# Optimization experiments

Hardware: AMD Instinct MI355X
Metric: run time of the kernel (lower is better)

Reference implementation:

```python
import jax, jax.numpy as jnp
import numpy as np

IH, IW = 32, 32
HEADS, DIM_HEAD = 8, 32
EPS = 1e-6


def conv3x3(x, w):
    # x: [B,C,H,W], w: [O,I,3,3], stride 1, pad 1, no bias
    return jax.lax.conv_general_dilated(x, w, (1, 1), ((1, 1), (1, 1)),
                                        dimension_numbers=('NCHW', 'OIHW', 'NCHW'))


def groupnorm1(x, g, b):
    # GroupNorm(1, C): normalize over (C,H,W) per sample
    mu = jnp.mean(x, axis=(1, 2, 3), keepdims=True)
    var = jnp.var(x, axis=(1, 2, 3), keepdims=True)
    xn = (x - mu) * jax.lax.rsqrt(var + EPS)
    return xn * g[None, :, None, None] + b[None, :, None, None]


def proj(x, w, g, b):
    return jax.nn.gelu(groupnorm1(conv3x3(x, w), g, b), approximate=False)


def relative_index(ih, iw):
    coords = np.stack(np.meshgrid(np.arange(ih), np.arange(iw), indexing='ij')).reshape(2, -1)
    rel = coords[:, :, None] - coords[:, None, :]  # [2, n, n]
    rel[0] += ih - 1
    rel[1] += iw - 1
    rel[0] *= 2 * iw - 1
    return jnp.asarray(rel.sum(0).reshape(-1))  # [n*n]


def setup_inputs() -> dict:
    key = jax.random.key(0)
    ks = jax.random.split(key, 9)
    C = HEADS * DIM_HEAD  # 256
    B = 8
    s = 0.02
    inp = {
        'x': jax.random.normal(ks[0], (B, C, IH, IW), jnp.float32),
        'wq': jax.random.normal(ks[1], (C, C, 3, 3), jnp.float32) * s,
        'wk': jax.random.normal(ks[2], (C, C, 3, 3), jnp.float32) * s,
        'wv': jax.random.normal(ks[3], (C, C, 3, 3), jnp.float32) * s,
        'gq': jnp.ones((C,), jnp.float32), 'bq': jnp.zeros((C,), jnp.float32),
        'gk': jnp.ones((C,), jnp.float32), 'bk': jnp.zeros((C,), jnp.float32),
        'gv': jnp.ones((C,), jnp.float32), 'bv': jnp.zeros((C,), jnp.float32),
        'bias_table': jax.random.normal(ks[4], ((2 * IH - 1) * (2 * IW - 1), HEADS), jnp.float32) * s,
        'wo': jax.random.normal(ks[5], (C, C), jnp.float32) * s,
        'bo': jnp.zeros((C,), jnp.float32),
    }
    return inp


def reference(x, wq, wk, wv, gq, bq, gk, bk, gv, bv, bias_table, wo, bo):
    B, C, ih, iw = x.shape
    n = ih * iw
    h, d = HEADS, DIM_HEAD

    q = proj(x, wq, gq, bq)  # [B,C,H,W]
    k = proj(x, wk, gk, bk)
    v = proj(x, wv, gv, bv)

    # 'b c ih iw -> b (ih iw) c' then 'b n (h d) -> b h n d'  ==  [B,h,d,n] -> [B,h,n,d]
    def to_heads(t):
        return t.reshape(B, h, d, n).transpose(0, 1, 3, 2)

    q4, k4, v4 = to_heads(q), to_heads(k), to_heads(v)

    # NOTE: original code applies self.scale only when y is not None; y=None here -> no scale.
    dots = jnp.einsum('bhnd,bhmd->bhnm', q4, k4)  # [B,h,n,n]

    rel_idx = relative_index(ih, iw)  # [n*n]
    rel_bias = bias_table[rel_idx].reshape(n, n, h).transpose(2, 0, 1)[None]  # [1,h,n,n]

    attn = jax.nn.softmax(dots + rel_bias, axis=-1)
    out = jnp.einsum('bhnm,bhmd->bhnd', attn, v4)  # [B,h,n,d]

    # 'b h n d -> b n (h d)' then 'b (ih iw) c -> b c ih iw'
    out = out.transpose(0, 2, 1, 3).reshape(B, n, C).transpose(0, 2, 1).reshape(B, C, ih, iw)

    # to_out: 1x1 conv with bias (dropout=0 in eval)
    out = jnp.einsum('oc,bchw->bohw', wo, out) + bo[None, :, None, None]
    return out
```

## Files before the change

### kernel.cpp

```cpp
#include <hip/hip_runtime.h>
#include <cstdint>
#include <cstddef>

#define GEPS 1e-6f

using bf16x8 = __attribute__((ext_vector_type(8))) short;
using f32x4  = __attribute__((ext_vector_type(4))) float;

__device__ inline ushort f2bf(float x) {
    union { float f; uint32_t u; } v; v.f = x;
    uint32_t r = (v.u + 0x7fffu + ((v.u >> 16) & 1u)) >> 16;
    return (ushort)r;
}

__device__ inline void gll16(const void* g, void* l) {
    __builtin_amdgcn_global_load_lds(
        (const __attribute__((address_space(1))) void*)g,
        (__attribute__((address_space(3))) void*)l, 16, 0, 0);
}

__global__ __launch_bounds__(256) void pack_k(
    const float* __restrict__ wq, const float* __restrict__ wk,
    const float* __restrict__ wv, const float* __restrict__ wo,
    const float* __restrict__ btab,
    ushort* __restrict__ Wbuf, ushort* __restrict__ wo_bf,
    float* __restrict__ bias_r)
{
    int blk = blockIdx.x, tid = threadIdx.x;
    if (blk < 768) {
        __shared__ ushort Ws[2304];
        int proj = blk >> 8, co = blk & 255;
        const float* src = ((proj == 0) ? wq : ((proj == 1) ? wk : wv)) + (size_t)co * 2304;
#pragma unroll
        for (int j = 0; j < 9; ++j) {
            int idx = j * 256 + tid;
            Ws[idx] = f2bf(src[idx]);
        }
        __syncthreads();
        ushort* dst = Wbuf + (size_t)blk * 2304;
#pragma unroll
        for (int j = 0; j < 9; ++j)
            dst[j * 256 + tid] = Ws[tid * 9 + j];
        return;
    }
    if (blk < 832) {
        int t = (blk - 768) * 256 + tid;
        float4 v = *(const float4*)&wo[(size_t)t * 4];
        union { uint2 u; ushort s[4]; } o;
        o.s[0] = f2bf(v.x); o.s[1] = f2bf(v.y); o.s[2] = f2bf(v.z); o.s[3] = f2bf(v.w);
        *(uint2*)&wo_bf[(size_t)t * 4] = o.u;
        return;
    }
    int t = (blk - 832) * 256 + tid;
    if (t < 8 * 3969) {
        int h = t / 3969, rk = t - h * 3969;
        bias_r[t] = btab[rk * 8 + h];
    }
}

__global__ __launch_bounds__(256) void im2col_k(const float* __restrict__ x,
                                                ushort* __restrict__ Ab)
{
    __shared__ __align__(16) ushort Xs[3 * 34 * 128];
    int tid = threadIdx.x;
    int blk = blockIdx.x;
    int b = blk >> 6, py = (blk >> 1) & 31, half = blk & 1;

#pragma unroll
    for (int p = tid; p < 768; p += 256) {
        int yy = p >> 8;
        int q = p & 255;
        int col = (q >> 7) ? 33 : 0;
        int ci = q & 127;
        Xs[(yy * 34 + col) * 128 + ci] = 0;
    }

#pragma unroll
    for (int it = 0; it < 12; ++it) {
        int j = it * 256 + tid;
        int ci_l = j / 24;
        int o = (j - ci_l * 24) * 4;
        int yy = o >> 5, xx = o & 31;
        int row = py - 1 + yy;
        float4 v = make_float4(0.f, 0.f, 0.f, 0.f);
        if (row >= 0 && row < 32)
            v = *(const float4*)&x[((size_t)(b * 256 + half * 128 + ci_l)) * 1024 + row * 32 + xx];
        int base = (yy * 34 + xx + 1) * 128 + ci_l;
        Xs[base + 0 * 128] = f2bf(v.x);
        Xs[base + 1 * 128] = f2bf(v.y);
        Xs[base + 2 * 128] = f2bf(v.z);
        Xs[base + 3 * 128] = f2bf(v.w);
    }
    __syncthreads();

    ushort* dst = Ab + (size_t)(b * 1024 + py * 32) * 2304;
#pragma unroll
    for (int it = 0; it < 18; ++it) {
        int idx = it * 256 + tid;
        int ci8l = idx & 15;
        int tp = (idx >> 4) % 9;
        int px = idx / 144;
        int kh = tp / 3, kw = tp - kh * 3;
        uint4 p = *(const uint4*)&Xs[(kh * 34 + px + kw) * 128 + ci8l * 8];
        *(uint4*)&dst[(size_t)(px * 288 + tp * 32 + half * 16 + ci8l) * 8] = p;
    }
}

__global__ __launch_bounds__(256, 3) void gemm_bt(
    const ushort* __restrict__ A, const ushort* __restrict__ B,
    int M, int N, int K,
    float* __restrict__ Cpart,
    float* __restrict__ Cout, const float* __restrict__ bias, int mode)
{
    __shared__ __align__(16) ushort As[128 * 64];
    __shared__ __align__(16) ushort Bs[128 * 64];
    int tid = threadIdx.x;
    int mbase = blockIdx.x * 128, nbase = blockIdx.y * 128;
    int kspan = K / gridDim.z;
    int k0 = blockIdx.z * kspan;
    int wave = tid >> 6, lane = tid & 63;
    int wm = wave & 1, wn = wave >> 1;
    int quad = lane >> 4, c = lane & 15;

    int row_s = tid >> 3;
    int cc8 = (tid & 7) ^ (row_s & 7);
    ushort* ldsA = As + wave * 512;
    ushort* ldsB = Bs + wave * 512;

    f32x4 acc[4][4];
#pragma unroll
    for (int i = 0; i < 4; ++i)
#pragma unroll
        for (int j = 0; j < 4; ++j) acc[i][j] = (f32x4){0.f, 0.f, 0.f, 0.f};

    for (int kb = k0; kb < k0 + kspan; kb += 64) {
        __syncthreads();
#pragma unroll
        for (int R = 0; R < 4; ++R) {
            int row = R * 32 + row_s;
            gll16(A + (size_t)(mbase + row) * K + kb + cc8 * 8,
                  ldsA + R * 2048);
            gll16(B + (size_t)(nbase + row) * K + kb + cc8 * 8,
                  ldsB + R * 2048);
        }
        __syncthreads();
#pragma unroll
        for (int kq = 0; kq < 2; ++kq) {
            bf16x8 af[4], bfr[4];
            int sw = ((kq * 4 + quad) ^ (c & 7)) * 8;
#pragma unroll
            for (int i = 0; i < 4; ++i) {
                af[i]  = *(const bf16x8*)&As[(wm * 64 + i * 16 + c) * 64 + sw];
                bfr[i] = *(const bf16x8*)&Bs[(wn * 64 + i * 16 + c) * 64 + sw];
            }
#pragma unroll
            for (int i = 0; i < 4; ++i)
#pragma unroll
                for (int j = 0; j < 4; ++j)
                    acc[i][j] = __builtin_amdgcn_mfma_f32_16x16x32_bf16(
                        af[i], bfr[j], acc[i][j], 0, 0, 0);
        }
    }

    if (mode == 0) {
        float* Cp = Cpart + (size_t)blockIdx.z * M * N;
#pragma unroll
        for (int i = 0; i < 4; ++i) {
            int mrow = mbase + wm * 64 + i * 16 + quad * 4;
#pragma unroll
            for (int j = 0; j < 4; ++j) {
                int ncol = nbase + wn * 64 + j * 16 + c;
#pragma unroll
                for (int r = 0; r < 4; ++r)
                    Cp[(size_t)(mrow + r) * N + ncol] = acc[i][j][r];
            }
        }
    } else {
#pragma unroll
        for (int i = 0; i < 4; ++i) {
            int mrow0 = mbase + wm * 64 + i * 16 + quad * 4;
#pragma unroll
            for (int j = 0; j < 4; ++j) {
                int ncol = nbase + wn * 64 + j * 16 + c;
                int bb = ncol >> 10, px = ncol & 1023;
#pragma unroll
                for (int r = 0; r < 4; ++r) {
                    int o = mrow0 + r;
                    Cout[((size_t)bb * 256 + o) * 1024 + px] = acc[i][j][r] + bias[o];
                }
            }
        }
    }
}

__global__ __launch_bounds__(256) void stats1_k(const float* __restrict__ P0,
                                                const float* __restrict__ P1,
                                                float2* __restrict__ part)
{
    int t = blockIdx.x * 256 + threadIdx.x;
    size_t base = (size_t)t * 8;
    float4 a0 = *(const float4*)&P0[base];
    float4 a1 = *(const float4*)&P0[base + 4];
    float4 c0 = *(const float4*)&P1[base];
    float4 c1 = *(const float4*)&P1[base + 4];
    float v[8] = {a0.x + c0.x, a0.y + c0.y, a0.z + c0.z, a0.w + c0.w,
                  a1.x + c1.x, a1.y + c1.y, a1.z + c1.z, a1.w + c1.w};
    float s1 = 0.f, s2 = 0.f;
#pragma unroll
    for (int e = 0; e < 8; ++e) { s1 += v[e]; s2 += v[e] * v[e]; }
#pragma unroll
    for (int mk = 1; mk < 32; mk <<= 1) {
        s1 += __shfl_xor(s1, mk, 64);
        s2 += __shfl_xor(s2, mk, 64);
    }
    if ((threadIdx.x & 31) == 0) {
        int gg = t >> 5;
        int m = gg / 3;
        int proj = gg - m * 3;
        int b = m >> 10, slot = m & 1023;
        part[(proj * 8 + b) * 1024 + slot] = make_float2(s1, s2);
    }
}

__global__ __launch_bounds__(256) void stats2_k(const float2* __restrict__ part,
                                                float* __restrict__ stats)
{
    __shared__ float w1[4], w2[4];
    int s = blockIdx.x, tid = threadIdx.x;
    float s1 = 0.f, s2 = 0.f;
#pragma unroll
    for (int i = 0; i < 4; ++i) {
        float2 v = part[(size_t)s * 1024 + tid * 4 + i];
        s1 += v.x; s2 += v.y;
    }
#pragma unroll
    for (int mk = 1; mk < 64; mk <<= 1) {
        s1 += __shfl_xor(s1, mk, 64);
        s2 += __shfl_xor(s2, mk, 64);
    }
    if ((tid & 63) == 0) { w1[tid >> 6] = s1; w2[tid >> 6] = s2; }
    __syncthreads();
    if (tid == 0) {
        stats[s * 2 + 0] = w1[0] + w1[1] + w1[2] + w1[3];
        stats[s * 2 + 1] = w2[0] + w2[1] + w2[2] + w2[3];
    }
}

__global__ void gn_k(const float* __restrict__ P0, const float* __restrict__ P1,
                     const float* __restrict__ stats,
                     const float* __restrict__ gq, const float* __restrict__ bq,
                     const float* __restrict__ gk, const float* __restrict__ bk,
                     const float* __restrict__ gv, const float* __restrict__ bv,
                     ushort* __restrict__ qb, ushort* __restrict__ kb2,
                     ushort* __restrict__ vt)
{
    int t = blockIdx.x * 256 + threadIdx.x;
    int m = t / 96;
    int nn = (t - m * 96) * 8;
    int proj = nn >> 8, co = nn & 255;
    int b = m >> 10, px = m & 1023;
    float s1 = stats[(proj * 8 + b) * 2 + 0];
    float s2 = stats[(proj * 8 + b) * 2 + 1];
    const float Ninv = 1.f / 262144.f;
    float mu = s1 * Ninv;
    float var = fmaxf(s2 * Ninv - mu * mu, 0.f);
    float rsig = rsqrtf(var + GEPS);
    const float* gam = (proj == 0) ? gq : ((proj == 1) ? gk : gv);
    const float* bet = (proj == 0) ? bq : ((proj == 1) ? bk : bv);

    size_t base = (size_t)m * 768 + nn;
    float4 a0 = *(const float4*)&P0[base];
    float4 a1 = *(const float4*)&P0[base + 4];
    float4 c0 = *(const float4*)&P1[base];
    float4 c1 = *(const float4*)&P1[base + 4];
    float xv[8] = {a0.x + c0.x, a0.y + c0.y, a0.z + c0.z, a0.w + c0.w,
                   a1.x + c1.x, a1.y + c1.y, a1.z + c1.z, a1.w + c1.w};
    union { uint4 v; ushort s[8]; } outp;
#pragma unroll
    for (int e = 0; e < 8; ++e) {
        int cc = co + e;
        float xn = (xv[e] - mu) * rsig * gam[cc] + bet[cc];
        float ge = 0.5f * xn * (1.f + erff(xn * 0.70710678118654752f));
        outp.s[e] = f2bf(ge);
    }
    int h = co >> 5, d = co & 31;
    if (proj == 0) {
        *(uint4*)(qb + ((((size_t)b * 8 + h) * 1024 + px) * 32 + d)) = outp.v;
    } else if (proj == 1) {
        *(uint4*)(kb2 + ((((size_t)b * 8 + h) * 1024 + px) * 32 + d)) = outp.v;
    } else {
#pragma unroll
        for (int e = 0; e < 8; ++e)
            vt[(((size_t)b * 8 + h) * 32 + d + e) * 1024 + px] = outp.s[e];
    }
}

__global__ __launch_bounds__(256, 2) void attn_k(
    const ushort* __restrict__ qb, const ushort* __restrict__ kb,
    const ushort* __restrict__ vt, const float* __restrict__ bias_r,
    ushort* __restrict__ attnout)
{
    __shared__ __align__(16) ushort Pl[4 * 16 * 72];
    int tid = threadIdx.x, wave = tid >> 6, lane = tid & 63;
    int quad = lane >> 4, c = lane & 15;
    int bh = blockIdx.y;
    int h = bh & 7, b = bh >> 3;
    int qbase = blockIdx.x * 64 + wave * 16;

    const ushort* Q  = qb + (size_t)bh * 1024 * 32;
    const ushort* Kp = kb + (size_t)bh * 1024 * 32;
    const ushort* Vt = vt + (size_t)bh * 32 * 1024;
    const float* brh = bias_r + h * 3969;
    ushort* Pw = Pl + wave * 16 * 72;

    bf16x8 qf = *(const bf16x8*)&Q[(qbase + c) * 32 + quad * 8];

    float l_[4] = {0.f, 0.f, 0.f, 0.f};
    f32x4 Of0 = {0.f, 0.f, 0.f, 0.f}, Of1 = {0.f, 0.f, 0.f, 0.f};
    int qy[4], qx[4];
#pragma unroll
    for (int r = 0; r < 4; ++r) {
        int qr = qbase + quad * 4 + r;
        qy[r] = qr >> 5; qx[r] = qr & 31;
    }

    for (int kb64 = 0; kb64 < 1024; kb64 += 64) {
        f32x4 S[4];
        f32x4 zf = {0.f, 0.f, 0.f, 0.f};
#pragma unroll
        for (int f = 0; f < 4; ++f) {
            bf16x8 kf = *(const bf16x8*)&Kp[(kb64 + f * 16 + c) * 32 + quad * 8];
            S[f] = __builtin_amdgcn_mfma_f32_16x16x32_bf16(qf, kf, zf, 0, 0, 0);
        }
#pragma unroll
        for (int f = 0; f < 4; ++f) {
            int key = kb64 + f * 16 + c;
            int ky = key >> 5, kx = key & 31;
#pragma unroll
            for (int r = 0; r < 4; ++r) {
                float p = __expf(S[f][r] + brh[(qy[r] - ky + 31) * 63 + (qx[r] - kx + 31)]);
                S[f][r] = p;
                l_[r] += p;
            }
        }
#pragma unroll
        for (int f = 0; f < 4; ++f)
#pragma unroll
            for (int r = 0; r < 4; ++r)
                Pw[(quad * 4 + r) * 72 + f * 16 + c] = f2bf(S[f][r]);
#pragma unroll
        for (int kc = 0; kc < 2; ++kc) {
            bf16x8 pf = *(const bf16x8*)&Pw[c * 72 + kc * 32 + quad * 8];
            bf16x8 vf0 = *(const bf16x8*)&Vt[(c) * 1024 + kb64 + kc * 32 + quad * 8];
            Of0 = __builtin_amdgcn_mfma_f32_16x16x32_bf16(pf, vf0, Of0, 0, 0, 0);
            bf16x8 vf1 = *(const bf16x8*)&Vt[(16 + c) * 1024 + kb64 + kc * 32 + quad * 8];
            Of1 = __builtin_amdgcn_mfma_f32_16x16x32_bf16(pf, vf1, Of1, 0, 0, 0);
        }
    }
#pragma unroll
    for (int r = 0; r < 4; ++r) {
        float l = l_[r];
        l += __shfl_xor(l, 1, 64);
        l += __shfl_xor(l, 2, 64);
        l += __shfl_xor(l, 4, 64);
        l += __shfl_xor(l, 8, 64);
        float inv = 1.f / l;
        int qr = qbase + quad * 4 + r;
        size_t base = ((size_t)b * 1024 + qr) * 256 + h * 32;
        attnout[base + c]      = f2bf(Of0[r] * inv);
        attnout[base + 16 + c] = f2bf(Of1[r] * inv);
    }
}

extern "C" void kernel_launch(void* const* d_in, const int* in_sizes, int n_in,
                              void* d_out, int out_size, void* d_ws, size_t ws_size,
                              hipStream_t stream)
{
    const float* x    = (const float*)d_in[0];
    const float* wq   = (const float*)d_in[1];
    const float* wk   = (const float*)d_in[2];
    const float* wv   = (const float*)d_in[3];
    const float* gq   = (const float*)d_in[4];
    const float* bq   = (const float*)d_in[5];
    const float* gk   = (const float*)d_in[6];
    const float* bk   = (const float*)d_in[7];
    const float* gv   = (const float*)d_in[8];
    const float* bv   = (const float*)d_in[9];
    const float* btab = (const float*)d_in[10];
    const float* wo   = (const float*)d_in[11];
    const float* bo   = (const float*)d_in[12];
    float* out = (float*)d_out;

    char* w = (char*)d_ws;
    size_t off = 0;
    auto alloc = [&](size_t bytes) -> char* {
        char* p = w + off;
        off += (bytes + 255) & ~(size_t)255;
        return p;
    };
    ushort* Abuf    = (ushort*)alloc(8192ull * 2304 * 2);
    ushort* Wbuf    = (ushort*)alloc(768ull * 2304 * 2);
    ushort* wo_bf   = (ushort*)alloc(65536ull * 2);
    float*  bias_r  = (float*)alloc(8ull * 3969 * 4);
    float*  P0      = (float*)alloc(8192ull * 768 * 4);
    float*  P1      = (float*)alloc(8192ull * 768 * 4);
    float2* part    = (float2*)alloc(48ull * 1024 * 8);
    float*  stats   = (float*)alloc(384);
    ushort* qb      = (ushort*)Abuf;
    ushort* kb2     = qb  + 8ull * 8 * 1024 * 32;
    ushort* vt      = kb2 + 8ull * 8 * 1024 * 32;
    ushort* attnout = vt  + 8ull * 8 * 32 * 1024;

    pack_k<<<957, 256, 0, stream>>>(wq, wk, wv, wo, btab, Wbuf, wo_bf, bias_r);
    im2col_k<<<512, 256, 0, stream>>>(x, Abuf);
    gemm_bt<<<dim3(64, 6, 2), 256, 0, stream>>>(Abuf, Wbuf, 8192, 768, 2304,
                                                P0, nullptr, nullptr, 0);
    stats1_k<<<3072, 256, 0, stream>>>(P0, P1, part);
    stats2_k<<<48, 256, 0, stream>>>(part, stats);
    gn_k<<<3072, 256, 0, stream>>>(P0, P1, stats, gq, bq, gk, bk, gv, bv,
                                   qb, kb2, vt);
    attn_k<<<dim3(16, 64), 256, 0, stream>>>(qb, kb2, vt, bias_r, attnout);
    gemm_bt<<<dim3(2, 64, 1), 256, 0, stream>>>(wo_bf, attnout, 256, 8192, 256,
                                                nullptr, out, bo, 1);
}
```

Before: 235.7 us.

## Pre-expand relative bias into MFMA fragment layout and swizzle V for coalesced loads

Adds a kernel that expands the relative-position bias table into a per-head bf16 tensor laid out exactly as each lane's MFMA accumulator fragment. The attention loop can then fetch its 16 bias values with two 16-byte loads instead of computing indices and gathering 16 scattered floats. The V projection is also written in a lane-swizzled fragment layout, so each B-operand load is one contiguous 16-byte read per lane. In exchange, the expanded bias is an extra ~16 MB written and read per call, and bias precision drops from fp32 to bf16.

Result: no change. 236.2 us (+0.2%).

```diff
diff --git a/kernel.cpp b/kernel.cpp
--- a/kernel.cpp
+++ b/kernel.cpp
@@ -12,6 +12,10 @@
     uint32_t r = (v.u + 0x7fffu + ((v.u >> 16) & 1u)) >> 16;
     return (ushort)r;
 }
+__device__ inline float bf2f(ushort b) {
+    union { float f; uint32_t u; } v; v.u = ((uint32_t)b) << 16;
+    return v.f;
+}
 
 __device__ inline void gll16(const void* g, void* l) {
     __builtin_amdgcn_global_load_lds(
@@ -22,9 +26,7 @@
 __global__ __launch_bounds__(256) void pack_k(
     const float* __restrict__ wq, const float* __restrict__ wk,
     const float* __restrict__ wv, const float* __restrict__ wo,
-    const float* __restrict__ btab,
-    ushort* __restrict__ Wbuf, ushort* __restrict__ wo_bf,
-    float* __restrict__ bias_r)
+    ushort* __restrict__ Wbuf, ushort* __restrict__ wo_bf)
 {
     int blk = blockIdx.x, tid = threadIdx.x;
     if (blk < 768) {
@@ -43,19 +45,34 @@
             dst[j * 256 + tid] = Ws[tid * 9 + j];
         return;
     }
-    if (blk < 832) {
-        int t = (blk - 768) * 256 + tid;
-        float4 v = *(const float4*)&wo[(size_t)t * 4];
-        union { uint2 u; ushort s[4]; } o;
-        o.s[0] = f2bf(v.x); o.s[1] = f2bf(v.y); o.s[2] = f2bf(v.z); o.s[3] = f2bf(v.w);
-        *(uint2*)&wo_bf[(size_t)t * 4] = o.u;
-        return;
-    }
-    int t = (blk - 832) * 256 + tid;
-    if (t < 8 * 3969) {
-        int h = t / 3969, rk = t - h * 3969;
-        bias_r[t] = btab[rk * 8 + h];
-    }
+    int t = (blk - 768) * 256 + tid;
+    float4 v = *(const float4*)&wo[(size_t)t * 4];
+    union { uint2 u; ushort s[4]; } o;
+    o.s[0] = f2bf(v.x); o.s[1] = f2bf(v.y); o.s[2] = f2bf(v.z); o.s[3] = f2bf(v.w);
+    *(uint2*)&wo_bf[(size_t)t * 4] = o.u;
+}
+
+__global__ __launch_bounds__(256) void bx_k(const float* __restrict__ btab,
+                                            ushort* __restrict__ Bx)
+{
+    int g = blockIdx.x * 4 + (threadIdx.x >> 6);
+    int l = threadIdx.x & 63;
+    int h = g >> 10, qt = (g >> 4) & 63, kt = g & 15;
+    int quad = l >> 4, c = l & 15;
+    union { uint4 v[2]; ushort s[16]; } o;
+#pragma unroll
+    for (int f = 0; f < 4; ++f)
+#pragma unroll
+        for (int r = 0; r < 4; ++r) {
+            int qrow = qt * 16 + quad * 4 + r;
+            int key = kt * 64 + f * 16 + c;
+            int dy = (qrow >> 5) - (key >> 5) + 31;
+            int dx = (qrow & 31) - (key & 31) + 31;
+            o.s[f * 4 + r] = f2bf(btab[(dy * 63 + dx) * 8 + h]);
+        }
+    uint4* dst = (uint4*)(Bx + ((size_t)g * 64 + l) * 16);
+    dst[0] = o.v[0];
+    dst[1] = o.v[1];
 }
 
 __global__ __launch_bounds__(256) void im2col_k(const float* __restrict__ x,
@@ -252,7 +269,7 @@
                      const float* __restrict__ gk, const float* __restrict__ bk,
                      const float* __restrict__ gv, const float* __restrict__ bv,
                      ushort* __restrict__ qb, ushort* __restrict__ kb2,
-                     ushort* __restrict__ vt)
+                     ushort* __restrict__ vx)
 {
     int t = blockIdx.x * 256 + threadIdx.x;
     int m = t / 96;
@@ -289,15 +306,19 @@
     } else if (proj == 1) {
         *(uint4*)(kb2 + ((((size_t)b * 8 + h) * 1024 + px) * 32 + d)) = outp.v;
     } else {
-#pragma unroll
-        for (int e = 0; e < 8; ++e)
-            vt[(((size_t)b * 8 + h) * 32 + d + e) * 1024 + px] = outp.s[e];
+        ushort* vb = vx + ((size_t)b * 8 + h) * 32768;
+        int kca = px >> 5, quad = (px >> 3) & 3, j = px & 7;
+#pragma unroll
+        for (int e = 0; e < 8; ++e) {
+            int dd = d + e;
+            vb[(((kca * 2 + (dd >> 4)) * 64) + quad * 16 + (dd & 15)) * 8 + j] = outp.s[e];
+        }
     }
 }
 
 __global__ __launch_bounds__(256, 2) void attn_k(
     const ushort* __restrict__ qb, const ushort* __restrict__ kb,
-    const ushort* __restrict__ vt, const float* __restrict__ bias_r,
+    const ushort* __restrict__ vx, const ushort* __restrict__ Bx,
     ushort* __restrict__ attnout)
 {
     __shared__ __align__(16) ushort Pl[4 * 16 * 72];
@@ -309,20 +330,14 @@
 
     const ushort* Q  = qb + (size_t)bh * 1024 * 32;
     const ushort* Kp = kb + (size_t)bh * 1024 * 32;
-    const ushort* Vt = vt + (size_t)bh * 32 * 1024;
-    const float* brh = bias_r + h * 3969;
+    const ushort* Vb = vx + (size_t)bh * 32768;
+    const ushort* bxp = Bx + (((size_t)(h * 64 + (qbase >> 4)) * 16) * 64 + lane) * 16;
     ushort* Pw = Pl + wave * 16 * 72;
 
     bf16x8 qf = *(const bf16x8*)&Q[(qbase + c) * 32 + quad * 8];
 
     float l_[4] = {0.f, 0.f, 0.f, 0.f};
     f32x4 Of0 = {0.f, 0.f, 0.f, 0.f}, Of1 = {0.f, 0.f, 0.f, 0.f};
-    int qy[4], qx[4];
-#pragma unroll
-    for (int r = 0; r < 4; ++r) {
-        int qr = qbase + quad * 4 + r;
-        qy[r] = qr >> 5; qx[r] = qr & 31;
-    }
 
     for (int kb64 = 0; kb64 < 1024; kb64 += 64) {
         f32x4 S[4];
@@ -332,17 +347,18 @@
             bf16x8 kf = *(const bf16x8*)&Kp[(kb64 + f * 16 + c) * 32 + quad * 8];
             S[f] = __builtin_amdgcn_mfma_f32_16x16x32_bf16(qf, kf, zf, 0, 0, 0);
         }
-#pragma unroll
-        for (int f = 0; f < 4; ++f) {
-            int key = kb64 + f * 16 + c;
-            int ky = key >> 5, kx = key & 31;
+        union { uint4 v[2]; ushort s[16]; } bu;
+        const uint4* bsrc = (const uint4*)(bxp + (size_t)(kb64 >> 6) * 1024);
+        bu.v[0] = bsrc[0];
+        bu.v[1] = bsrc[1];
+#pragma unroll
+        for (int f = 0; f < 4; ++f)
 #pragma unroll
             for (int r = 0; r < 4; ++r) {
-                float p = __expf(S[f][r] + brh[(qy[r] - ky + 31) * 63 + (qx[r] - kx + 31)]);
+                float p = __expf(S[f][r] + bf2f(bu.s[f * 4 + r]));
                 S[f][r] = p;
                 l_[r] += p;
             }
-        }
 #pragma unroll
         for (int f = 0; f < 4; ++f)
 #pragma unroll
@@ -350,10 +366,11 @@
                 Pw[(quad * 4 + r) * 72 + f * 16 + c] = f2bf(S[f][r]);
 #pragma unroll
         for (int kc = 0; kc < 2; ++kc) {
+            int kca = (kb64 >> 5) + kc;
             bf16x8 pf = *(const bf16x8*)&Pw[c * 72 + kc * 32 + quad * 8];
-            bf16x8 vf0 = *(const bf16x8*)&Vt[(c) * 1024 + kb64 + kc * 32 + quad * 8];
+            bf16x8 vf0 = *(const bf16x8*)&Vb[((kca * 2 + 0) * 64 + lane) * 8];
             Of0 = __builtin_amdgcn_mfma_f32_16x16x32_bf16(pf, vf0, Of0, 0, 0, 0);
-            bf16x8 vf1 = *(const bf16x8*)&Vt[(16 + c) * 1024 + kb64 + kc * 32 + quad * 8];
+            bf16x8 vf1 = *(const bf16x8*)&Vb[((kca * 2 + 1) * 64 + lane) * 8];
             Of1 = __builtin_amdgcn_mfma_f32_16x16x32_bf16(pf, vf1, Of1, 0, 0, 0);
         }
     }
@@ -401,25 +418,26 @@
     ushort* Abuf    = (ushort*)alloc(8192ull * 2304 * 2);
     ushort* Wbuf    = (ushort*)alloc(768ull * 2304 * 2);
     ushort* wo_bf   = (ushort*)alloc(65536ull * 2);
-    float*  bias_r  = (float*)alloc(8ull * 3969 * 4);
     float*  P0      = (float*)alloc(8192ull * 768 * 4);
     float*  P1      = (float*)alloc(8192ull * 768 * 4);
     float2* part    = (float2*)alloc(48ull * 1024 * 8);
     float*  stats   = (float*)alloc(384);
     ushort* qb      = (ushort*)Abuf;
     ushort* kb2     = qb  + 8ull * 8 * 1024 * 32;
-    ushort* vt      = kb2 + 8ull * 8 * 1024 * 32;
-    ushort* attnout = vt  + 8ull * 8 * 32 * 1024;
-
-    pack_k<<<957, 256, 0, stream>>>(wq, wk, wv, wo, btab, Wbuf, wo_bf, bias_r);
+    ushort* vx      = kb2 + 8ull * 8 * 1024 * 32;
+    ushort* attnout = vx  + 8ull * 8 * 32 * 1024;
+    ushort* Bx      = attnout + 8192ull * 256;
+
+    pack_k<<<832, 256, 0, stream>>>(wq, wk, wv, wo, Wbuf, wo_bf);
     im2col_k<<<512, 256, 0, stream>>>(x, Abuf);
     gemm_bt<<<dim3(64, 6, 2), 256, 0, stream>>>(Abuf, Wbuf, 8192, 768, 2304,
                                                 P0, nullptr, nullptr, 0);
+    bx_k<<<2048, 256, 0, stream>>>(btab, Bx);
     stats1_k<<<3072, 256, 0, stream>>>(P0, P1, part);
     stats2_k<<<48, 256, 0, stream>>>(part, stats);
     gn_k<<<3072, 256, 0, stream>>>(P0, P1, stats, gq, bq, gk, bk, gv, bv,
-                                   qb, kb2, vt);
-    attn_k<<<dim3(16, 64), 256, 0, stream>>>(qb, kb2, vt, bias_r, attnout);
+                                   qb, kb2, vx);
+    attn_k<<<dim3(16, 64), 256, 0, stream>>>(qb, kb2, vx, Bx, attnout);
     gemm_bt<<<dim3(2, 64, 1), 256, 0, stream>>>(wo_bf, attnout, 256, 8192, 256,
                                                 nullptr, out, bo, 1);
 }
```
